# Kernel tuning notes

Hardware: AMD Instinct MI355X
Metric: run time of the kernel (lower is better)

The kernel has to match this reference:

```python
import jax, jax.numpy as jnp
import numpy as np

B, T, S, A, P = 256, 32, 2048, 64, 128


def setup_inputs() -> dict:
    key = jax.random.key(0)
    ks = jax.random.split(key, 10)
    def w(k, shape, fan_in):
        return jax.random.normal(k, shape, dtype=jnp.float32) / np.sqrt(fan_in)
    return {
        "state": jax.random.normal(ks[0], (B, S), dtype=jnp.float32),
        "act_sequence": jax.random.normal(ks[1], (B, T, A), dtype=jnp.float32),
        "latent": jax.random.normal(ks[2], (B, P), dtype=jnp.float32),
        "fc_W": w(ks[3], (S, S + A + P), S + A + P),
        "fc_b": jnp.zeros((S,), dtype=jnp.float32),
        "fc1_W": w(ks[4], (S, 2 * S), 2 * S),
        "fc2_W": w(ks[5], (S, S), S),
        "W_W": w(ks[6], (4 * S, S), S),
        "reward_W": w(ks[7], (1, S), S),
        "reward_b": jnp.zeros((1,), dtype=jnp.float32),
    }


def reference(state, act_sequence, latent, fc_W, fc_b, fc1_W, fc2_W, W_W, reward_W, reward_b):
    s_dim = fc2_W.shape[0]
    relu = jax.nn.relu

    def fc(x):  # nn.Linear(s+a+p -> s, bias=True)
        return x @ fc_W.T + fc_b

    # initial hidden/cell both from relu(fc(cat[state, act[:,0], latent]))
    hs0 = jnp.concatenate([state, act_sequence[:, 0, :], latent], axis=1)
    hidden = relu(fc(hs0))
    cell = relu(fc(hs0))

    acts = jnp.transpose(act_sequence, (1, 0, 2))  # [T, B, A]

    def step(carry, act_i):
        h, c = carry
        # LSTMCell called as lstm(hidden, [hidden, cell]) -> input == h_cur == h
        combined = jnp.concatenate([h, h], axis=1)            # [B, 2S]
        x = relu(combined @ fc1_W.T)
        x = relu(x @ fc2_W.T)
        cc = relu(x @ W_W.T)                                   # [B, 4S]
        cc_i, cc_f, cc_o, cc_g = jnp.split(cc, 4, axis=1)
        i_g = jax.nn.sigmoid(cc_i)
        f_g = jax.nn.sigmoid(cc_f)
        o_g = jax.nn.sigmoid(cc_o)
        g_g = jnp.tanh(cc_g)
        c_next = f_g * c + i_g * g_g
        h_next = o_g * jnp.tanh(c_next)
        reward = h_next @ reward_W.T + reward_b                # [B, 1]
        # hidden for next iteration (uses act_sequence[:, i, :], as in source);
        # at the last step this carry is simply discarded.
        hs = jnp.concatenate([h_next, act_i, latent], axis=1)
        h_carry = relu(fc(hs))
        return (h_carry, c_next), (h_next, reward)

    (_, _), (preds, rewards) = jax.lax.scan(step, (hidden, cell), acts)
    # torch.cat(list, dim=0) over T steps of [B, *] -> [T*B, *]
    preds = preds.reshape(-1, s_dim)
    rewards = rewards.reshape(-1, 1)
    return preds, rewards
```

## Files before the change

### kernel.cpp

```cpp
#include <hip/hip_runtime.h>

typedef unsigned short u16;
typedef unsigned int   u32;
typedef __attribute__((ext_vector_type(8))) short s8v;
typedef __attribute__((ext_vector_type(8))) unsigned short u8v;
typedef __attribute__((ext_vector_type(4))) float f32x4;

__device__ __forceinline__ float bf2f(u16 v) {
    union { u32 u; float f; } x; x.u = ((u32)v) << 16; return x.f;
}
__device__ __forceinline__ u16 f2bf(float f) {
    union { float f; u32 u; } x; x.f = f;
    return (u16)((x.u + 0x7fffu + ((x.u >> 16) & 1u)) >> 16);
}
__device__ __forceinline__ float sigf(float x)  { return 1.0f / (1.0f + __expf(-x)); }
__device__ __forceinline__ float tanhf_(float x){ return 1.0f - 2.0f / (__expf(2.0f * x) + 1.0f); }

constexpr int Bb = 256, Tt = 32, Ss = 2048, Aa = 64, Pp = 128, SAPd = 2240;

typedef const __attribute__((address_space(1))) unsigned int* gp1_t;
typedef __attribute__((address_space(3))) unsigned int* lp3_t;
__device__ __forceinline__ void gl16(const void* g, void* l) {
    __builtin_amdgcn_global_load_lds((gp1_t)g, (lp3_t)l, 16, 0, 0);
}
#define VMW3() asm volatile("s_waitcnt vmcnt(3)" ::: "memory")
#define VMW0() asm volatile("s_waitcnt vmcnt(0)" ::: "memory")

template<int NBXPX, int NBY>
__device__ __forceinline__ void xcd_decode(int& bx, int& by) {
    int id  = blockIdx.x;
    int xcd = id & 7, i = id >> 3;
    bx = xcd * NBXPX + (i & (NBXPX - 1));
    by = i / NBXPX;
}

__global__ void detect_k(const u32* __restrict__ st, int* __restrict__ flag) {
    u32 w = st[threadIdx.x];
    int e = (w >> 7) & 0xFF;
    unsigned long long m = __ballot(e >= 100 && e <= 140);
    if (threadIdx.x == 0) flag[0] = (__popcll(m) >= 32) ? 1 : 0;
}

__global__ __launch_bounds__(256)
void prep_k(const void* __restrict__ state, const void* __restrict__ act,
            const void* __restrict__ latent, const void* __restrict__ fc1W,
            u16* __restrict__ hs, u16* __restrict__ fc1s, float* __restrict__ rewbuf,
            const int* __restrict__ flagp, int big)
{
    const bool bfe = (flagp[0] == 1);
    int g0 = blockIdx.x * 256 + threadIdx.x;
    int stride = gridDim.x * 256;
    for (int i = g0; i < Bb * SAPd; i += stride) {
        int b = i / SAPd, k = i - b * SAPd;
        const void* p; size_t src;
        if (k < Ss)           { p = state;  src = (size_t)b * Ss + k; }
        else if (k < Ss + Aa) { p = act;    src = (size_t)b * (Tt * Aa) + (k - Ss); }
        else                  { p = latent; src = (size_t)b * Pp + (k - Ss - Aa); }
        hs[i] = bfe ? ((const u16*)p)[src] : f2bf(((const float*)p)[src]);
    }
    for (int i = g0; i < Tt * Bb; i += stride) rewbuf[i] = 0.0f;
    if (big) {
        for (int i = g0; i < Ss * Ss; i += stride) {
            int n = i >> 11, k = i & 2047;
            float s;
            if (bfe) s = bf2f(((const u16*)fc1W)[(size_t)n * 4096 + k])
                       + bf2f(((const u16*)fc1W)[(size_t)n * 4096 + 2048 + k]);
            else     s = ((const float*)fc1W)[(size_t)n * 4096 + k]
                       + ((const float*)fc1W)[(size_t)n * 4096 + 2048 + k];
            fc1s[i] = f2bf(s);
        }
    }
}

template<int K, bool BIAS, bool WC, bool FOLD, bool ACT, bool WBF>
__global__ __launch_bounds__(256)
void gemm_k(const u16* __restrict__ Ap, const void* __restrict__ Wp,
            const void* __restrict__ biasp, u16* __restrict__ outp,
            float* __restrict__ cellp,
            u16* __restrict__ hsp, const void* __restrict__ actp, int t,
            const int* __restrict__ flagp)
{
    constexpr int NK = K / 64;
    __shared__ __align__(16) char smem[36864];
    const bool bfe = (flagp[0] == 1);
    const int tid = threadIdx.x;
    const int lane = tid & 63, w = tid >> 6, m16 = lane & 15, q = lane >> 4;
    int bx, by; xcd_decode<4, 8>(bx, by);
    const int r0 = by * 32, c0 = bx * 64;

    if (ACT) {
        if (by == 0) {
            int i = bx * 512 + tid * 2;
            int b = i >> 6, a2 = i & 63;
            if (bfe) {
                u32 v = *(const u32*)((const u16*)actp + ((size_t)b * Tt + t) * Aa + a2);
                *(u32*)(hsp + (size_t)b * SAPd + Ss + a2) = v;
            } else {
                const float* s = (const float*)actp + ((size_t)b * Tt + t) * Aa + a2;
                *(u32*)(hsp + (size_t)b * SAPd + Ss + a2) =
                    (u32)f2bf(s[0]) | ((u32)f2bf(s[1]) << 16);
            }
            VMW0();
        }
    }

    const int srow = tid >> 3, sch = tid & 7;
    const int fr2 = 32 + srow;
    f32x4 acc0 = {}, acc1 = {};
    const bool mainp = (WBF || bfe) && !FOLD;

    auto COMPUTE = [&](int p) {
        const char* bufA = smem + p * 12288;
        const char* bufB = bufA + 4096;
        const int sw = (m16 & 7) << 4;
        #pragma unroll
        for (int kh = 0; kh < 2; kh++) {
            int cb = ((kh << 6) | (q << 4)) ^ sw;
            s8v b  = *(const s8v*)(bufB + (w * 16 + m16) * 128 + cb);
            s8v a0 = *(const s8v*)(bufA + m16 * 128 + cb);
            s8v a1 = *(const s8v*)(bufA + (16 + m16) * 128 + cb);
            acc0 = __builtin_amdgcn_mfma_f32_16x16x32_bf16(a0, b, acc0, 0, 0, 0);
            acc1 = __builtin_amdgcn_mfma_f32_16x16x32_bf16(a1, b, acc1, 0, 0, 0);
        }
    };

    if (mainp) {
        const u16* W16 = (const u16*)Wp;
        auto STAGE = [&](int kt, int p) {
            char* bufA = smem + p * 12288;
            char* bufB = bufA + 4096;
            int kb = kt * 64;
            gl16(Ap + (size_t)(r0 + srow) * K + kb + ((sch ^ (srow & 7)) * 8),
                 bufA + w * 1024);
            gl16(W16 + (size_t)(c0 + srow) * K + kb + ((sch ^ (srow & 7)) * 8),
                 bufB + w * 1024);
            gl16(W16 + (size_t)(c0 + fr2) * K + kb + ((sch ^ (fr2 & 7)) * 8),
                 bufB + 4096 + w * 1024);
        };
        STAGE(0, 0); STAGE(1, 1);
        for (int k = 0; k < NK - 2; k++) {
            VMW3();
            __builtin_amdgcn_s_barrier();
            STAGE(k + 2, (k + 2) % 3);
            COMPUTE(k % 3);
        }
        VMW3();
        __builtin_amdgcn_s_barrier();
        COMPUTE((NK - 2) % 3);
        VMW0();
        __builtin_amdgcn_s_barrier();
        COMPUTE((NK - 1) % 3);
    } else {
        u8v fa; u8v rbh[4]; float4 rff[8];
        auto ISSUE = [&](int kt) {
            int kb = kt * 64;
            fa = *(const u8v*)(Ap + (size_t)(r0 + srow) * K + kb + sch * 8);
            if (FOLD) {
                if (bfe) {
                    const u16* p1 = (const u16*)Wp + (size_t)(c0 + srow) * (2 * K) + kb + sch * 8;
                    rbh[0] = *(const u8v*)p1; rbh[1] = *(const u8v*)(p1 + K);
                    const u16* p2 = (const u16*)Wp + (size_t)(c0 + fr2) * (2 * K) + kb + sch * 8;
                    rbh[2] = *(const u8v*)p2; rbh[3] = *(const u8v*)(p2 + K);
                } else {
                    const float* p1 = (const float*)Wp + (size_t)(c0 + srow) * (2 * K) + kb + sch * 8;
                    rff[0] = *(const float4*)p1;       rff[1] = *(const float4*)(p1 + 4);
                    rff[2] = *(const float4*)(p1 + K); rff[3] = *(const float4*)(p1 + K + 4);
                    const float* p2 = (const float*)Wp + (size_t)(c0 + fr2) * (2 * K) + kb + sch * 8;
                    rff[4] = *(const float4*)p2;       rff[5] = *(const float4*)(p2 + 4);
                    rff[6] = *(const float4*)(p2 + K); rff[7] = *(const float4*)(p2 + K + 4);
                }
            } else {
                const float* p1 = (const float*)Wp + (size_t)(c0 + srow) * K + kb + sch * 8;
                rff[0] = *(const float4*)p1; rff[1] = *(const float4*)(p1 + 4);
                const float* p2 = (const float*)Wp + (size_t)(c0 + fr2) * K + kb + sch * 8;
                rff[2] = *(const float4*)p2; rff[3] = *(const float4*)(p2 + 4);
            }
        };
        auto COMMIT = [&](int p) {
            char* bufA = smem + p * 12288;
            char* bufB = bufA + 4096;
            *(u8v*)(bufA + srow * 128 + ((sch ^ (srow & 7)) * 16)) = fa;
            u8v v1, v2;
            if (FOLD) {
                if (bfe) {
                    #pragma unroll
                    for (int j = 0; j < 8; j++) {
                        v1[j] = f2bf(bf2f(rbh[0][j]) + bf2f(rbh[1][j]));
                        v2[j] = f2bf(bf2f(rbh[2][j]) + bf2f(rbh[3][j]));
                    }
                } else {
                    float a0[8], a1[8], b0[8], b1[8];
                    *(float4*)&a0[0] = rff[0]; *(float4*)&a0[4] = rff[1];
                    *(float4*)&a1[0] = rff[2]; *(float4*)&a1[4] = rff[3];
                    *(float4*)&b0[0] = rff[4]; *(float4*)&b0[4] = rff[5];
                    *(float4*)&b1[0] = rff[6]; *(float4*)&b1[4] = rff[7];
                    #pragma unroll
                    for (int j = 0; j < 8; j++) {
                        v1[j] = f2bf(a0[j] + a1[j]);
                        v2[j] = f2bf(b0[j] + b1[j]);
                    }
                }
            } else {
                float a0[8], a1[8];
                *(float4*)&a0[0] = rff[0]; *(float4*)&a0[4] = rff[1];
                *(float4*)&a1[0] = rff[2]; *(float4*)&a1[4] = rff[3];
                #pragma unroll
                for (int j = 0; j < 8; j++) { v1[j] = f2bf(a0[j]); v2[j] = f2bf(a1[j]); }
            }
            *(u8v*)(bufB + srow * 128 + ((sch ^ (srow & 7)) * 16)) = v1;
            *(u8v*)(bufB + fr2 * 128 + ((sch ^ (fr2 & 7)) * 16)) = v2;
        };
        ISSUE(0);
        for (int k = 0; k < NK; k++) {
            __syncthreads();
            COMMIT(k & 1);
            __syncthreads();
            if (k + 1 < NK) ISSUE(k + 1);
            COMPUTE(k & 1);
        }
    }

    const int col = c0 + w * 16 + m16;
    float bv = 0.0f;
    if (BIAS) bv = bfe ? bf2f(((const u16*)biasp)[col]) : ((const float*)biasp)[col];
    #pragma unroll
    for (int r = 0; r < 4; r++) {
        int row0 = r0 + q * 4 + r;
        float v0 = fmaxf(acc0[r] + bv, 0.0f);
        outp[(size_t)row0 * 2048 + col] = f2bf(v0);
        if (WC) cellp[(size_t)row0 * 2048 + col] = v0;
        int row1 = r0 + 16 + q * 4 + r;
        float v1 = fmaxf(acc1[r] + bv, 0.0f);
        outp[(size_t)row1 * 2048 + col] = f2bf(v1);
        if (WC) cellp[(size_t)row1 * 2048 + col] = v1;
    }
}

__global__ __launch_bounds__(256)
void wgates_k(const u16* __restrict__ Ap, const void* __restrict__ Wp,
              float* __restrict__ cbuf, u16* __restrict__ hsp,
              void* __restrict__ dout, const void* __restrict__ rwWp,
              float* __restrict__ rewbuf, int t, const int* __restrict__ flagp)
{
    constexpr int K = 2048, NK = 32;
    __shared__ __align__(16) char smem[36864];
    const bool bfe = (flagp[0] == 1);
    const int tid = threadIdx.x;
    const int lane = tid & 63, g = tid >> 6, m16 = lane & 15, q = lane >> 4;
    int bx, by; xcd_decode<16, 8>(bx, by);
    const int r0 = by * 32, j0 = bx * 16;

    const int srow = tid >> 3, sch = tid & 7;
    const int fr2 = 32 + srow;
    const int wr1 = (srow >> 4) * 2048 + j0 + (srow & 15);
    const int wr2 = (fr2 >> 4) * 2048 + j0 + (fr2 & 15);
    f32x4 acc0 = {}, acc1 = {};

    auto COMPUTE = [&](int p) {
        const char* bufA = smem + p * 12288;
        const char* bufB = bufA + 4096;
        const int sw = (m16 & 7) << 4;
        #pragma unroll
        for (int kh = 0; kh < 2; kh++) {
            int cb = ((kh << 6) | (q << 4)) ^ sw;
            s8v b  = *(const s8v*)(bufB + (g * 16 + m16) * 128 + cb);
            s8v a0 = *(const s8v*)(bufA + m16 * 128 + cb);
            s8v a1 = *(const s8v*)(bufA + (16 + m16) * 128 + cb);
            acc0 = __builtin_amdgcn_mfma_f32_16x16x32_bf16(a0, b, acc0, 0, 0, 0);
            acc1 = __builtin_amdgcn_mfma_f32_16x16x32_bf16(a1, b, acc1, 0, 0, 0);
        }
    };

    if (bfe) {
        const u16* W16 = (const u16*)Wp;
        auto STAGE = [&](int kt, int p) {
            char* bufA = smem + p * 12288;
            char* bufB = bufA + 4096;
            int kb = kt * 64;
            gl16(Ap + (size_t)(r0 + srow) * K + kb + ((sch ^ (srow & 7)) * 8),
                 bufA + g * 1024);
            gl16(W16 + (size_t)wr1 * K + kb + ((sch ^ (srow & 7)) * 8),
                 bufB + g * 1024);
            gl16(W16 + (size_t)wr2 * K + kb + ((sch ^ (fr2 & 7)) * 8),
                 bufB + 4096 + g * 1024);
        };
        STAGE(0, 0); STAGE(1, 1);
        for (int k = 0; k < NK - 2; k++) {
            VMW3();
            __builtin_amdgcn_s_barrier();
            STAGE(k + 2, (k + 2) % 3);
            COMPUTE(k % 3);
        }
        VMW3();
        __builtin_amdgcn_s_barrier();
        COMPUTE((NK - 2) % 3);
        VMW0();
        __builtin_amdgcn_s_barrier();
        COMPUTE((NK - 1) % 3);
    } else {
        u8v fa; float4 rff[4];
        auto ISSUE = [&](int kt) {
            int kb = kt * 64;
            fa = *(const u8v*)(Ap + (size_t)(r0 + srow) * K + kb + sch * 8);
            const float* p1 = (const float*)Wp + (size_t)wr1 * K + kb + sch * 8;
            rff[0] = *(const float4*)p1; rff[1] = *(const float4*)(p1 + 4);
            const float* p2 = (const float*)Wp + (size_t)wr2 * K + kb + sch * 8;
            rff[2] = *(const float4*)p2; rff[3] = *(const float4*)(p2 + 4);
        };
        auto COMMIT = [&](int p) {
            char* bufA = smem + p * 12288;
            char* bufB = bufA + 4096;
            *(u8v*)(bufA + srow * 128 + ((sch ^ (srow & 7)) * 16)) = fa;
            float a0[8], a1[8];
            *(float4*)&a0[0] = rff[0]; *(float4*)&a0[4] = rff[1];
            *(float4*)&a1[0] = rff[2]; *(float4*)&a1[4] = rff[3];
            u8v v1, v2;
            #pragma unroll
            for (int j = 0; j < 8; j++) { v1[j] = f2bf(a0[j]); v2[j] = f2bf(a1[j]); }
            *(u8v*)(bufB + srow * 128 + ((sch ^ (srow & 7)) * 16)) = v1;
            *(u8v*)(bufB + fr2 * 128 + ((sch ^ (fr2 & 7)) * 16)) = v2;
        };
        ISSUE(0);
        for (int k = 0; k < NK; k++) {
            __syncthreads();
            COMMIT(k & 1);
            __syncthreads();
            if (k + 1 < NK) ISSUE(k + 1);
            COMPUTE(k & 1);
        }
    }

    __syncthreads();
    float* gbuf = (float*)smem;
    #pragma unroll
    for (int r = 0; r < 4; r++) {
        int row0 = q * 4 + r;
        gbuf[(row0 * 16 + m16) * 4 + g] = fmaxf(acc0[r], 0.0f);
        int row1 = 16 + q * 4 + r;
        gbuf[(row1 * 16 + m16) * 4 + g] = fmaxf(acc1[r], 0.0f);
    }
    __syncthreads();

    const int row = tid >> 3, jj = (tid & 7) * 2;
    const int grow = r0 + row, jcol = j0 + jj;
    float2 cold = *(const float2*)&cbuf[(size_t)grow * 2048 + jcol];
    float rw0 = bfe ? bf2f(((const u16*)rwWp)[jcol])     : ((const float*)rwWp)[jcol];
    float rw1 = bfe ? bf2f(((const u16*)rwWp)[jcol + 1]) : ((const float*)rwWp)[jcol + 1];

    float cn[2], hnf[2];
    float coldv[2] = { cold.x, cold.y };
    float rsum = 0.0f;
    #pragma unroll
    for (int u = 0; u < 2; u++) {
        const float* gq = &gbuf[((row * 16) + jj + u) * 4];
        float ig = sigf(gq[0]), fg = sigf(gq[1]), og = sigf(gq[2]), tg = tanhf_(gq[3]);
        float c_ = fg * coldv[u] + ig * tg;
        float hn = og * tanhf_(c_);
        cn[u] = c_; hnf[u] = hn;
        rsum += hn * (u ? rw1 : rw0);
    }
    *(float2*)&cbuf[(size_t)grow * 2048 + jcol] = *(float2*)cn;
    u32 hpack = (u32)f2bf(hnf[0]) | ((u32)f2bf(hnf[1]) << 16);
    *(u32*)&hsp[(size_t)grow * SAPd + jcol] = hpack;
    size_t pb = ((size_t)t * 256 + grow) * 2048 + jcol;
    if (bfe) *(u32*)&((u16*)dout)[pb] = hpack;
    else     { ((float*)dout)[pb] = hnf[0]; ((float*)dout)[pb + 1] = hnf[1]; }

    rsum += __shfl_xor(rsum, 1);
    rsum += __shfl_xor(rsum, 2);
    rsum += __shfl_xor(rsum, 4);
    if ((tid & 7) == 0) atomicAdd(&rewbuf[t * 256 + grow], rsum);
}

__global__ void rewfin_k(const float* __restrict__ rewbuf, void* __restrict__ dout,
                         const void* __restrict__ rwb, const int* __restrict__ flagp) {
    const bool bfe = (flagp[0] == 1);
    int i = blockIdx.x * 256 + threadIdx.x;
    float rb = bfe ? bf2f(((const u16*)rwb)[0]) : ((const float*)rwb)[0];
    float v = rewbuf[i] + rb;
    size_t o = (size_t)Tt * Bb * Ss + i;
    if (bfe) ((u16*)dout)[o] = f2bf(v);
    else     ((float*)dout)[o] = v;
}

extern "C" void kernel_launch(void* const* d_in, const int* in_sizes, int n_in,
                              void* d_out, int out_size, void* d_ws, size_t ws_size,
                              hipStream_t stream)
{
    const void* state  = d_in[0];
    const void* act    = d_in[1];
    const void* latent = d_in[2];
    const void* fcW    = d_in[3];
    const void* fcb    = d_in[4];
    const void* fc1W   = d_in[5];
    const void* fc2W   = d_in[6];
    const void* WW     = d_in[7];
    const void* rwW    = d_in[8];
    const void* rwb    = d_in[9];
    char* ws = (char*)d_ws;

    int*   flag   = (int*)  (ws + 0);
    u16*   hs     = (u16*)  (ws + 1024);
    u16*   h      = (u16*)  (ws + 1147904);
    u16*   x1     = (u16*)  (ws + 2196480);
    u16*   x2     = (u16*)  (ws + 3245056);
    float* cbuf   = (float*)(ws + 4293632);
    float* rewbuf = (float*)(ws + 6390784);
    u16*   fc1s   = (u16*)  (ws + 6423552);
    const bool big = ws_size >= 14812160ull;

    detect_k<<<dim3(1), dim3(64), 0, stream>>>((const u32*)state, flag);
    prep_k<<<dim3(4096), dim3(256), 0, stream>>>(state, act, latent, fc1W,
                                                 hs, fc1s, rewbuf, flag, big ? 1 : 0);

    gemm_k<2240, true, true, false, false, false><<<dim3(256), dim3(256), 0, stream>>>(
        hs, fcW, fcb, h, cbuf, nullptr, nullptr, 0, flag);

    for (int t = 0; t < 32; t++) {
        if (big)
            gemm_k<2048, false, false, false, true, true><<<dim3(256), dim3(256), 0, stream>>>(
                h, fc1s, nullptr, x1, nullptr, hs, act, t, flag);
        else
            gemm_k<2048, false, false, true, true, false><<<dim3(256), dim3(256), 0, stream>>>(
                h, fc1W, nullptr, x1, nullptr, hs, act, t, flag);
        gemm_k<2048, false, false, false, false, false><<<dim3(256), dim3(256), 0, stream>>>(
            x1, fc2W, nullptr, x2, nullptr, nullptr, nullptr, 0, flag);
        wgates_k<<<dim3(1024), dim3(256), 0, stream>>>(
            x2, WW, cbuf, hs, d_out, rwW, rewbuf, t, flag);
        if (t < 31)
            gemm_k<2240, true, false, false, false, false><<<dim3(256), dim3(256), 0, stream>>>(
                hs, fcW, fcb, h, nullptr, nullptr, nullptr, 0, flag);
    }
    rewfin_k<<<dim3(32), dim3(256), 0, stream>>>(rewbuf, d_out, rwb, flag);
}
```

Measured before the change: 3.037 ms.

## Split K across warp pairs and enlarge wgates row tile with LDS reduction

The GEMM kernels now have each pair of warps cover half of every 64-wide K chunk, so each warp computes 2x2 MFMA fragments instead of 1x2. The halves are summed through an extra LDS buffer before the epilogue. wgates_k moves to 64-row tiles with half as many blocks, so each weight tile staged in shared memory is reused across twice as many batch rows, and its epilogue handles 4 columns per thread. The cost is more shared memory, an extra barrier and reduction pass, and fewer blocks in flight for the gates kernel.

```diff
diff --git a/kernel.cpp b/kernel.cpp
--- a/kernel.cpp
+++ b/kernel.cpp
@@ -4,6 +4,7 @@
 typedef unsigned int   u32;
 typedef __attribute__((ext_vector_type(8))) short s8v;
 typedef __attribute__((ext_vector_type(8))) unsigned short u8v;
+typedef __attribute__((ext_vector_type(4))) unsigned short u4h;
 typedef __attribute__((ext_vector_type(4))) float f32x4;
 
 __device__ __forceinline__ float bf2f(u16 v) {
@@ -23,8 +24,7 @@
 __device__ __forceinline__ void gl16(const void* g, void* l) {
     __builtin_amdgcn_global_load_lds((gp1_t)g, (lp3_t)l, 16, 0, 0);
 }
-#define VMW3() asm volatile("s_waitcnt vmcnt(3)" ::: "memory")
-#define VMW0() asm volatile("s_waitcnt vmcnt(0)" ::: "memory")
+#define VMWAIT(n) asm volatile("s_waitcnt vmcnt(" #n ")" ::: "memory")
 
 template<int NBXPX, int NBY>
 __device__ __forceinline__ void xcd_decode(int& bx, int& by) {
@@ -81,10 +81,11 @@
             const int* __restrict__ flagp)
 {
     constexpr int NK = K / 64;
-    __shared__ __align__(16) char smem[36864];
+    __shared__ __align__(16) char smem[36864 + 8192];
     const bool bfe = (flagp[0] == 1);
     const int tid = threadIdx.x;
     const int lane = tid & 63, w = tid >> 6, m16 = lane & 15, q = lane >> 4;
+    const int ct = w & 1, khw = w >> 1;
     int bx, by; xcd_decode<4, 8>(bx, by);
     const int r0 = by * 32, c0 = bx * 64;
 
@@ -100,28 +101,28 @@
                 *(u32*)(hsp + (size_t)b * SAPd + Ss + a2) =
                     (u32)f2bf(s[0]) | ((u32)f2bf(s[1]) << 16);
             }
-            VMW0();
+            VMWAIT(0);
         }
     }
 
     const int srow = tid >> 3, sch = tid & 7;
     const int fr2 = 32 + srow;
-    f32x4 acc0 = {}, acc1 = {};
+    f32x4 acc[4] = {};
     const bool mainp = (WBF || bfe) && !FOLD;
 
     auto COMPUTE = [&](int p) {
         const char* bufA = smem + p * 12288;
         const char* bufB = bufA + 4096;
         const int sw = (m16 & 7) << 4;
-        #pragma unroll
-        for (int kh = 0; kh < 2; kh++) {
-            int cb = ((kh << 6) | (q << 4)) ^ sw;
-            s8v b  = *(const s8v*)(bufB + (w * 16 + m16) * 128 + cb);
-            s8v a0 = *(const s8v*)(bufA + m16 * 128 + cb);
-            s8v a1 = *(const s8v*)(bufA + (16 + m16) * 128 + cb);
-            acc0 = __builtin_amdgcn_mfma_f32_16x16x32_bf16(a0, b, acc0, 0, 0, 0);
-            acc1 = __builtin_amdgcn_mfma_f32_16x16x32_bf16(a1, b, acc1, 0, 0, 0);
-        }
+        const int cb = ((khw << 6) | (q << 4)) ^ sw;
+        s8v a0 = *(const s8v*)(bufA + m16 * 128 + cb);
+        s8v a1 = *(const s8v*)(bufA + (16 + m16) * 128 + cb);
+        s8v b0 = *(const s8v*)(bufB + (ct * 32 + m16) * 128 + cb);
+        s8v b1 = *(const s8v*)(bufB + (ct * 32 + 16 + m16) * 128 + cb);
+        acc[0] = __builtin_amdgcn_mfma_f32_16x16x32_bf16(a0, b0, acc[0], 0, 0, 0);
+        acc[1] = __builtin_amdgcn_mfma_f32_16x16x32_bf16(a1, b0, acc[1], 0, 0, 0);
+        acc[2] = __builtin_amdgcn_mfma_f32_16x16x32_bf16(a0, b1, acc[2], 0, 0, 0);
+        acc[3] = __builtin_amdgcn_mfma_f32_16x16x32_bf16(a1, b1, acc[3], 0, 0, 0);
     };
 
     if (mainp) {
@@ -139,15 +140,15 @@
         };
         STAGE(0, 0); STAGE(1, 1);
         for (int k = 0; k < NK - 2; k++) {
-            VMW3();
+            VMWAIT(3);
             __builtin_amdgcn_s_barrier();
             STAGE(k + 2, (k + 2) % 3);
             COMPUTE(k % 3);
         }
-        VMW3();
+        VMWAIT(3);
         __builtin_amdgcn_s_barrier();
         COMPUTE((NK - 2) % 3);
-        VMW0();
+        VMWAIT(0);
         __builtin_amdgcn_s_barrier();
         COMPUTE((NK - 1) % 3);
     } else {
@@ -220,19 +221,32 @@
         }
     }
 
-    const int col = c0 + w * 16 + m16;
-    float bv = 0.0f;
-    if (BIAS) bv = bfe ? bf2f(((const u16*)biasp)[col]) : ((const float*)biasp)[col];
-    #pragma unroll
-    for (int r = 0; r < 4; r++) {
-        int row0 = r0 + q * 4 + r;
-        float v0 = fmaxf(acc0[r] + bv, 0.0f);
-        outp[(size_t)row0 * 2048 + col] = f2bf(v0);
-        if (WC) cellp[(size_t)row0 * 2048 + col] = v0;
-        int row1 = r0 + 16 + q * 4 + r;
-        float v1 = fmaxf(acc1[r] + bv, 0.0f);
-        outp[(size_t)row1 * 2048 + col] = f2bf(v1);
-        if (WC) cellp[(size_t)row1 * 2048 + col] = v1;
+    f32x4* red = (f32x4*)(smem + 36864);
+    if (khw == 1) {
+        #pragma unroll
+        for (int f = 0; f < 4; f++) red[(ct * 4 + f) * 64 + lane] = acc[f];
+    }
+    __syncthreads();
+    if (khw == 0) {
+        #pragma unroll
+        for (int f = 0; f < 4; f++) acc[f] += red[(ct * 4 + f) * 64 + lane];
+        #pragma unroll
+        for (int cf = 0; cf < 2; cf++) {
+            const int col = c0 + ct * 32 + cf * 16 + m16;
+            float bv = 0.0f;
+            if (BIAS) bv = bfe ? bf2f(((const u16*)biasp)[col]) : ((const float*)biasp)[col];
+            #pragma unroll
+            for (int af = 0; af < 2; af++) {
+                f32x4 a = acc[cf * 2 + af];
+                #pragma unroll
+                for (int r = 0; r < 4; r++) {
+                    int row = r0 + af * 16 + q * 4 + r;
+                    float v = fmaxf(a[r] + bv, 0.0f);
+                    outp[(size_t)row * 2048 + col] = f2bf(v);
+                    if (WC) cellp[(size_t)row * 2048 + col] = v;
+                }
+            }
+        }
     }
 }
 
@@ -243,133 +257,171 @@
               float* __restrict__ rewbuf, int t, const int* __restrict__ flagp)
 {
     constexpr int K = 2048, NK = 32;
-    __shared__ __align__(16) char smem[36864];
+    __shared__ __align__(16) char smem[49152];
     const bool bfe = (flagp[0] == 1);
     const int tid = threadIdx.x;
-    const int lane = tid & 63, g = tid >> 6, m16 = lane & 15, q = lane >> 4;
-    int bx, by; xcd_decode<16, 8>(bx, by);
-    const int r0 = by * 32, j0 = bx * 16;
-
-    const int srow = tid >> 3, sch = tid & 7;
-    const int fr2 = 32 + srow;
-    const int wr1 = (srow >> 4) * 2048 + j0 + (srow & 15);
-    const int wr2 = (fr2 >> 4) * 2048 + j0 + (fr2 & 15);
-    f32x4 acc0 = {}, acc1 = {};
+    const int lane = tid & 63, w = tid >> 6, m16 = lane & 15, q = lane >> 4;
+    const int mi = w & 1, khw = w >> 1;
+    int bx, by; xcd_decode<16, 4>(bx, by);
+    const int r0 = by * 64, j0 = bx * 16;
+
+    const int srow8 = lane >> 3, sch = lane & 7;
+    f32x4 acc[8] = {};
 
     auto COMPUTE = [&](int p) {
-        const char* bufA = smem + p * 12288;
-        const char* bufB = bufA + 4096;
+        const char* bufA = smem + p * 16384;
+        const char* bufB = bufA + 8192;
         const int sw = (m16 & 7) << 4;
-        #pragma unroll
-        for (int kh = 0; kh < 2; kh++) {
-            int cb = ((kh << 6) | (q << 4)) ^ sw;
-            s8v b  = *(const s8v*)(bufB + (g * 16 + m16) * 128 + cb);
-            s8v a0 = *(const s8v*)(bufA + m16 * 128 + cb);
-            s8v a1 = *(const s8v*)(bufA + (16 + m16) * 128 + cb);
-            acc0 = __builtin_amdgcn_mfma_f32_16x16x32_bf16(a0, b, acc0, 0, 0, 0);
-            acc1 = __builtin_amdgcn_mfma_f32_16x16x32_bf16(a1, b, acc1, 0, 0, 0);
+        const int cb = ((khw << 6) | (q << 4)) ^ sw;
+        s8v a0 = *(const s8v*)(bufA + (mi * 32 + m16) * 128 + cb);
+        s8v a1 = *(const s8v*)(bufA + (mi * 32 + 16 + m16) * 128 + cb);
+        #pragma unroll
+        for (int cf = 0; cf < 4; cf++) {
+            s8v b = *(const s8v*)(bufB + (cf * 16 + m16) * 128 + cb);
+            acc[cf * 2 + 0] = __builtin_amdgcn_mfma_f32_16x16x32_bf16(a0, b, acc[cf * 2 + 0], 0, 0, 0);
+            acc[cf * 2 + 1] = __builtin_amdgcn_mfma_f32_16x16x32_bf16(a1, b, acc[cf * 2 + 1], 0, 0, 0);
         }
     };
 
     if (bfe) {
         const u16* W16 = (const u16*)Wp;
         auto STAGE = [&](int kt, int p) {
-            char* bufA = smem + p * 12288;
-            char* bufB = bufA + 4096;
+            char* bufA = smem + p * 16384;
+            char* bufB = bufA + 8192;
             int kb = kt * 64;
-            gl16(Ap + (size_t)(r0 + srow) * K + kb + ((sch ^ (srow & 7)) * 8),
-                 bufA + g * 1024);
-            gl16(W16 + (size_t)wr1 * K + kb + ((sch ^ (srow & 7)) * 8),
-                 bufB + g * 1024);
-            gl16(W16 + (size_t)wr2 * K + kb + ((sch ^ (fr2 & 7)) * 8),
-                 bufB + 4096 + g * 1024);
+            #pragma unroll
+            for (int i = 0; i < 2; i++) {
+                int s = w * 2 + i;
+                int row = s * 8 + srow8;
+                int cg = sch ^ (row & 7);
+                gl16(Ap + (size_t)(r0 + row) * K + kb + cg * 8, bufA + s * 1024);
+            }
+            #pragma unroll
+            for (int i = 0; i < 2; i++) {
+                int s = w * 2 + i;
+                int row = s * 8 + srow8;
+                int wr = (row >> 4) * 2048 + j0 + (row & 15);
+                int cg = sch ^ (row & 7);
+                gl16(W16 + (size_t)wr * K + kb + cg * 8, bufB + s * 1024);
+            }
         };
         STAGE(0, 0); STAGE(1, 1);
         for (int k = 0; k < NK - 2; k++) {
-            VMW3();
+            VMWAIT(4);
             __builtin_amdgcn_s_barrier();
             STAGE(k + 2, (k + 2) % 3);
             COMPUTE(k % 3);
         }
-        VMW3();
+        VMWAIT(4);
         __builtin_amdgcn_s_barrier();
         COMPUTE((NK - 2) % 3);
-        VMW0();
+        VMWAIT(0);
         __builtin_amdgcn_s_barrier();
         COMPUTE((NK - 1) % 3);
     } else {
-        u8v fa; float4 rff[4];
+        float4 rff[4];
         auto ISSUE = [&](int kt) {
             int kb = kt * 64;
-            fa = *(const u8v*)(Ap + (size_t)(r0 + srow) * K + kb + sch * 8);
-            const float* p1 = (const float*)Wp + (size_t)wr1 * K + kb + sch * 8;
-            rff[0] = *(const float4*)p1; rff[1] = *(const float4*)(p1 + 4);
-            const float* p2 = (const float*)Wp + (size_t)wr2 * K + kb + sch * 8;
-            rff[2] = *(const float4*)p2; rff[3] = *(const float4*)(p2 + 4);
+            #pragma unroll
+            for (int i = 0; i < 2; i++) {
+                int slot = tid + i * 256;
+                int brow = slot >> 3, bch = slot & 7;
+                int wr = (brow >> 4) * 2048 + j0 + (brow & 15);
+                int cg = bch ^ (brow & 7);
+                const float* p1 = (const float*)Wp + (size_t)wr * K + kb + cg * 8;
+                rff[2 * i] = *(const float4*)p1; rff[2 * i + 1] = *(const float4*)(p1 + 4);
+            }
+        };
+        auto STAGE_A = [&](int kt, int p) {
+            char* bufA = smem + p * 16384;
+            int kb = kt * 64;
+            #pragma unroll
+            for (int i = 0; i < 2; i++) {
+                int s = w * 2 + i;
+                int row = s * 8 + srow8;
+                int cg = sch ^ (row & 7);
+                gl16(Ap + (size_t)(r0 + row) * K + kb + cg * 8, bufA + s * 1024);
+            }
         };
         auto COMMIT = [&](int p) {
-            char* bufA = smem + p * 12288;
-            char* bufB = bufA + 4096;
-            *(u8v*)(bufA + srow * 128 + ((sch ^ (srow & 7)) * 16)) = fa;
-            float a0[8], a1[8];
-            *(float4*)&a0[0] = rff[0]; *(float4*)&a0[4] = rff[1];
-            *(float4*)&a1[0] = rff[2]; *(float4*)&a1[4] = rff[3];
-            u8v v1, v2;
-            #pragma unroll
-            for (int j = 0; j < 8; j++) { v1[j] = f2bf(a0[j]); v2[j] = f2bf(a1[j]); }
-            *(u8v*)(bufB + srow * 128 + ((sch ^ (srow & 7)) * 16)) = v1;
-            *(u8v*)(bufB + fr2 * 128 + ((sch ^ (fr2 & 7)) * 16)) = v2;
-        };
-        ISSUE(0);
+            char* bufB = smem + p * 16384 + 8192;
+            #pragma unroll
+            for (int i = 0; i < 2; i++) {
+                int slot = tid + i * 256;
+                int brow = slot >> 3, bch = slot & 7;
+                float a0[8];
+                *(float4*)&a0[0] = rff[2 * i]; *(float4*)&a0[4] = rff[2 * i + 1];
+                u8v v;
+                #pragma unroll
+                for (int j = 0; j < 8; j++) v[j] = f2bf(a0[j]);
+                *(u8v*)(bufB + brow * 128 + bch * 16) = v;
+            }
+        };
+        ISSUE(0); STAGE_A(0, 0);
         for (int k = 0; k < NK; k++) {
             __syncthreads();
             COMMIT(k & 1);
             __syncthreads();
-            if (k + 1 < NK) ISSUE(k + 1);
+            if (k + 1 < NK) { STAGE_A(k + 1, (k + 1) & 1); ISSUE(k + 1); }
             COMPUTE(k & 1);
         }
     }
 
+    f32x4* red = (f32x4*)(smem + 32768);
+    if (khw == 1) {
+        #pragma unroll
+        for (int f = 0; f < 8; f++) red[(mi * 8 + f) * 64 + lane] = acc[f];
+    }
     __syncthreads();
-    float* gbuf = (float*)smem;
+    float* gbuf = (float*)(smem + 32768);
+    if (khw == 0) {
+        #pragma unroll
+        for (int f = 0; f < 8; f++) acc[f] += red[(mi * 8 + f) * 64 + lane];
+        #pragma unroll
+        for (int af = 0; af < 2; af++)
+            #pragma unroll
+            for (int r = 0; r < 4; r++) {
+                int row = mi * 32 + af * 16 + q * 4 + r;
+                f32x4 gv;
+                #pragma unroll
+                for (int cf = 0; cf < 4; cf++) gv[cf] = fmaxf(acc[cf * 2 + af][r], 0.0f);
+                ((f32x4*)gbuf)[row * 16 + m16] = gv;
+            }
+    }
+    __syncthreads();
+
+    const int row = tid >> 2, jq = (tid & 3) * 4;
+    const int grow = r0 + row, jcol = j0 + jq;
+    float4 cold = *(const float4*)&cbuf[(size_t)grow * 2048 + jcol];
+    float coldv[4] = { cold.x, cold.y, cold.z, cold.w };
+    float rw4[4];
     #pragma unroll
-    for (int r = 0; r < 4; r++) {
-        int row0 = q * 4 + r;
-        gbuf[(row0 * 16 + m16) * 4 + g] = fmaxf(acc0[r], 0.0f);
-        int row1 = 16 + q * 4 + r;
-        gbuf[(row1 * 16 + m16) * 4 + g] = fmaxf(acc1[r], 0.0f);
-    }
-    __syncthreads();
-
-    const int row = tid >> 3, jj = (tid & 7) * 2;
-    const int grow = r0 + row, jcol = j0 + jj;
-    float2 cold = *(const float2*)&cbuf[(size_t)grow * 2048 + jcol];
-    float rw0 = bfe ? bf2f(((const u16*)rwWp)[jcol])     : ((const float*)rwWp)[jcol];
-    float rw1 = bfe ? bf2f(((const u16*)rwWp)[jcol + 1]) : ((const float*)rwWp)[jcol + 1];
-
-    float cn[2], hnf[2];
-    float coldv[2] = { cold.x, cold.y };
+    for (int u = 0; u < 4; u++)
+        rw4[u] = bfe ? bf2f(((const u16*)rwWp)[jcol + u]) : ((const float*)rwWp)[jcol + u];
+
+    float cn[4], hnf[4]; u4h hv;
     float rsum = 0.0f;
     #pragma unroll
-    for (int u = 0; u < 2; u++) {
-        const float* gq = &gbuf[((row * 16) + jj + u) * 4];
+    for (int u = 0; u < 4; u++) {
+        const float* gq = &gbuf[((row * 16) + jq + u) * 4];
         float ig = sigf(gq[0]), fg = sigf(gq[1]), og = sigf(gq[2]), tg = tanhf_(gq[3]);
         float c_ = fg * coldv[u] + ig * tg;
         float hn = og * tanhf_(c_);
-        cn[u] = c_; hnf[u] = hn;
-        rsum += hn * (u ? rw1 : rw0);
-    }
-    *(float2*)&cbuf[(size_t)grow * 2048 + jcol] = *(float2*)cn;
-    u32 hpack = (u32)f2bf(hnf[0]) | ((u32)f2bf(hnf[1]) << 16);
-    *(u32*)&hsp[(size_t)grow * SAPd + jcol] = hpack;
+        cn[u] = c_; hnf[u] = hn; hv[u] = f2bf(hn);
+        rsum += hn * rw4[u];
+    }
+    *(float4*)&cbuf[(size_t)grow * 2048 + jcol] = *(float4*)cn;
+    *(u4h*)&hsp[(size_t)grow * SAPd + jcol] = hv;
     size_t pb = ((size_t)t * 256 + grow) * 2048 + jcol;
-    if (bfe) *(u32*)&((u16*)dout)[pb] = hpack;
-    else     { ((float*)dout)[pb] = hnf[0]; ((float*)dout)[pb + 1] = hnf[1]; }
+    if (bfe) *(u4h*)&((u16*)dout)[pb] = hv;
+    else {
+        #pragma unroll
+        for (int u = 0; u < 4; u++) ((float*)dout)[pb + u] = hnf[u];
+    }
 
     rsum += __shfl_xor(rsum, 1);
     rsum += __shfl_xor(rsum, 2);
-    rsum += __shfl_xor(rsum, 4);
-    if ((tid & 7) == 0) atomicAdd(&rewbuf[t * 256 + grow], rsum);
+    if ((tid & 3) == 0) atomicAdd(&rewbuf[t * 256 + grow], rsum);
 }
 
 __global__ void rewfin_k(const float* __restrict__ rewbuf, void* __restrict__ dout,
@@ -425,7 +477,7 @@
                 h, fc1W, nullptr, x1, nullptr, hs, act, t, flag);
         gemm_k<2048, false, false, false, false, false><<<dim3(256), dim3(256), 0, stream>>>(
             x1, fc2W, nullptr, x2, nullptr, nullptr, nullptr, 0, flag);
-        wgates_k<<<dim3(1024), dim3(256), 0, stream>>>(
+        wgates_k<<<dim3(512), dim3(256), 0, stream>>>(
             x2, WW, cbuf, hs, d_out, rwW, rewbuf, t, flag);
         if (t < 31)
             gemm_k<2240, true, false, false, false, false><<<dim3(256), dim3(256), 0, stream>>>(
```

After: 2.708 ms. -10.8%, faster.
